# Kernel optimization log

Measured on AMD Instinct MI355X. Metric: run time of the kernel, lower is better.

## Reference

```python
import jax, jax.numpy as jnp
import numpy as np

PS = 32
D = 256


def setup_inputs() -> dict:
    key = jax.random.key(0)
    ks = jax.random.split(key, 9)
    B, L = 32, 32768
    s_in = 1.0 / np.sqrt(PS)
    s_d = 1.0 / np.sqrt(D)
    return {
        "x": jax.random.normal(ks[0], (B, L), dtype=jnp.float32),
        "W_proj": jax.random.normal(ks[1], (PS, D), dtype=jnp.float32) * s_in,
        "b_proj": jnp.zeros((D,), jnp.float32),
        "W_qkv": jax.random.normal(ks[2], (D, 3 * D), dtype=jnp.float32) * s_d,
        "b_qkv": jnp.zeros((3 * D,), jnp.float32),
        "W_out": jax.random.normal(ks[3], (D, D), dtype=jnp.float32) * s_d,
        "b_out": jnp.zeros((D,), jnp.float32),
        "W_head": jax.random.normal(ks[4], (D, PS), dtype=jnp.float32) * s_d,
        "b_head": jnp.zeros((PS,), jnp.float32),
    }


def reference(x, W_proj, b_proj, W_qkv, b_qkv, W_out, b_out, W_head, b_head):
    B, L = x.shape
    T = L // PS
    # InstanceNorm over full series (torch .std is unbiased -> ddof=1)
    mean = jnp.mean(x, axis=-1, keepdims=True)
    std = jnp.std(x, axis=-1, keepdims=True, ddof=1) + 1e-5
    x_norm = (x - mean) / std
    patches = x_norm.reshape(B, T, PS)
    # Patch embedding
    h = patches @ W_proj + b_proj  # [B, T, D]
    # Single-head causal self-attention (explicit scores, as in source)
    qkv = h @ W_qkv + b_qkv
    q, k, v = jnp.split(qkv, 3, axis=-1)
    scale = 1.0 / jnp.sqrt(jnp.asarray(D, dtype=h.dtype))
    attn = jnp.einsum("btd,bsd->bts", q, k) * scale  # [B, T, T]
    causal = jnp.tril(jnp.ones((T, T), dtype=bool))
    attn = jnp.where(causal, attn, -jnp.inf)
    attn = jax.nn.softmax(attn, axis=-1)
    out = jnp.einsum("bts,bsd->btd", attn, v)
    out = out @ W_out + b_out
    # Prediction head + next-patch MSE loss
    pred = out @ W_head + b_head  # [B, T, PS]
    loss = jnp.mean((pred[:, :-1] - patches[:, 1:]) ** 2)
    return loss
```

## Files before the change

kernel.cpp:

```cpp
#include <hip/hip_runtime.h>
#include <hip/hip_cooperative_groups.h>
#include <math.h>

namespace cg = cooperative_groups;

#define B_SZ 32
#define L_SZ 32768
#define T_SZ 1024
#define PS_SZ 32
#define D_SZ 256
#define SM_M 10.0f

typedef float f32x4 __attribute__((ext_vector_type(4)));
typedef short s16x8 __attribute__((ext_vector_type(8)));
typedef unsigned short u16x8 __attribute__((ext_vector_type(8)));

__device__ __forceinline__ unsigned short f2bf(float f) {
  union { float f; unsigned int u; } v; v.f = f;
  unsigned int r = v.u + 0x7FFFu + ((v.u >> 16) & 1u);
  return (unsigned short)(r >> 16);
}

__device__ __forceinline__ void g2l16(const unsigned short* g, unsigned short* l) {
  __builtin_amdgcn_global_load_lds(
      (const __attribute__((address_space(1))) unsigned int*)g,
      (__attribute__((address_space(3))) unsigned int*)l, 16, 0, 0);
}


__device__ __forceinline__ void phaseA_stats(const float* x, float* sgpart, int g, int tid,
                                             int w, int lane, float* red) {
  const int b = g >> 3;
  const float* p = x + (size_t)b * L_SZ + (size_t)(g & 7) * 4096;
  float s = 0.f, ss = 0.f;
#pragma unroll
  for (int i = 0; i < 4; ++i) {
    float4 f = ((const float4*)p)[tid + i * 256];
    s += f.x + f.y + f.z + f.w;
    ss += f.x * f.x + f.y * f.y + f.z * f.z + f.w * f.w;
  }
#pragma unroll
  for (int off = 32; off >= 1; off >>= 1) {
    s += __shfl_down(s, off);
    ss += __shfl_down(ss, off);
  }
  if (lane == 0) { red[w] = s; red[4 + w] = ss; }
  __syncthreads();
  if (tid == 0) {
    sgpart[g * 2]     = red[0] + red[1] + red[2] + red[3];
    sgpart[g * 2 + 1] = red[4] + red[5] + red[6] + red[7];
  }
  __syncthreads();
}

__device__ __forceinline__ void phaseA_folds(int idx, const float* Wp, const float* bp,
                                             const float* Wq, const float* bq,
                                             const float* Wo, const float* bo,
                                             const float* Wh, const float* bh,
                                             float* Wcb, unsigned short* WqT,
                                             unsigned short* WfT, float* bfp) {
  if (idx < 33 * 768) {
    int p = idx / 768, j = idx % 768;
    const float* arow = (p < 32) ? (Wp + p * 256) : bp;
    float acc = (p < 32) ? 0.f : bq[j];
    for (int d = 0; d < 256; ++d) acc += arow[d] * Wq[d * 768 + j];
    if (p < 32) WqT[j * 32 + p] = f2bf(acc);
    else Wcb[j] = acc;
  } else {
    int k = idx - 33 * 768;
    if (k < 8192) {
      int p = k >> 8, d = k & 255;
      float acc = 0.f;
      for (int e = 0; e < 256; ++e) acc += Wo[d * 256 + e] * Wh[e * 32 + p];
      WfT[p * 256 + d] = f2bf(acc);
    } else if (k < 8224) {
      int p = k - 8192;
      float acc = bh[p];
      for (int e = 0; e < 256; ++e) acc += bo[e] * Wh[e * 32 + p];
      bfp[p] = acc;
    }
  }
}

__device__ __forceinline__ void qkv_wave(const float* x, const float* sgpart,
                                         const unsigned short* WqT, const float* Wcb,
                                         unsigned short* Qb, unsigned short* Kb,
                                         unsigned short* Vtt, unsigned short* Tw,
                                         int mbase, int lane, int lo, int quad) {
  const int b = mbase >> 10;
  float S = 0.f, SS = 0.f;
#pragma unroll
  for (int i = 0; i < 8; ++i) {
    S += sgpart[(b * 8 + i) * 2];
    SS += sgpart[(b * 8 + i) * 2 + 1];
  }
  const float mean = S * (1.f / (float)L_SZ);
  const float var = (SS - S * mean) * (1.f / (float)(L_SZ - 1));
  const float inv = 1.f / (sqrtf(var) + 1e-5f);
  s16x8 af0, af1;
  {
    float4 a = *(const float4*)&x[(size_t)(mbase + lo) * 32 + quad * 8];
    float4 c = *(const float4*)&x[(size_t)(mbase + lo) * 32 + quad * 8 + 4];
    af0[0] = (short)f2bf((a.x - mean) * inv); af0[1] = (short)f2bf((a.y - mean) * inv);
    af0[2] = (short)f2bf((a.z - mean) * inv); af0[3] = (short)f2bf((a.w - mean) * inv);
    af0[4] = (short)f2bf((c.x - mean) * inv); af0[5] = (short)f2bf((c.y - mean) * inv);
    af0[6] = (short)f2bf((c.z - mean) * inv); af0[7] = (short)f2bf((c.w - mean) * inv);
    float4 d = *(const float4*)&x[(size_t)(mbase + 16 + lo) * 32 + quad * 8];
    float4 e = *(const float4*)&x[(size_t)(mbase + 16 + lo) * 32 + quad * 8 + 4];
    af1[0] = (short)f2bf((d.x - mean) * inv); af1[1] = (short)f2bf((d.y - mean) * inv);
    af1[2] = (short)f2bf((d.z - mean) * inv); af1[3] = (short)f2bf((d.w - mean) * inv);
    af1[4] = (short)f2bf((e.x - mean) * inv); af1[5] = (short)f2bf((e.y - mean) * inv);
    af1[6] = (short)f2bf((e.z - mean) * inv); af1[7] = (short)f2bf((e.w - mean) * inv);
  }
#pragma unroll 4
  for (int nt = 0; nt < 16; ++nt) {
    s16x8 bf = *(const s16x8*)&WqT[(size_t)(nt * 16 + lo) * 32 + quad * 8];
    f32x4 c0 = {0.f, 0.f, 0.f, 0.f}, c1 = {0.f, 0.f, 0.f, 0.f};
    c0 = __builtin_amdgcn_mfma_f32_16x16x32_bf16(af0, bf, c0, 0, 0, 0);
    c1 = __builtin_amdgcn_mfma_f32_16x16x32_bf16(af1, bf, c1, 0, 0, 0);
    const int col = nt * 16 + lo;
    const float bi = Wcb[col];
#pragma unroll
    for (int i = 0; i < 4; ++i) {
      Tw[(quad * 4 + i) * 264 + col]      = f2bf((c0[i] + bi) * 0.0625f);
      Tw[(16 + quad * 4 + i) * 264 + col] = f2bf((c1[i] + bi) * 0.0625f);
    }
  }
#pragma unroll
  for (int it = 0; it < 16; ++it) {
    const int gsub = it * 64 + lane;
    const int row = gsub >> 5, c16 = gsub & 31;
    *(u16x8*)&Qb[(size_t)(mbase + row) * 256 + c16 * 8] =
        *(const u16x8*)&Tw[row * 264 + c16 * 8];
  }
#pragma unroll 4
  for (int nt = 0; nt < 16; ++nt) {
    s16x8 bf = *(const s16x8*)&WqT[(size_t)(256 + nt * 16 + lo) * 32 + quad * 8];
    f32x4 c0 = {0.f, 0.f, 0.f, 0.f}, c1 = {0.f, 0.f, 0.f, 0.f};
    c0 = __builtin_amdgcn_mfma_f32_16x16x32_bf16(af0, bf, c0, 0, 0, 0);
    c1 = __builtin_amdgcn_mfma_f32_16x16x32_bf16(af1, bf, c1, 0, 0, 0);
    const int col = nt * 16 + lo;
    const float bi = Wcb[256 + col];
#pragma unroll
    for (int i = 0; i < 4; ++i) {
      Tw[(quad * 4 + i) * 264 + col]      = f2bf(c0[i] + bi);
      Tw[(16 + quad * 4 + i) * 264 + col] = f2bf(c1[i] + bi);
    }
  }
#pragma unroll
  for (int it = 0; it < 16; ++it) {
    const int gsub = it * 64 + lane;
    const int row = gsub >> 5, c16 = gsub & 31;
    *(u16x8*)&Kb[(size_t)(mbase + row) * 256 + c16 * 8] =
        *(const u16x8*)&Tw[row * 264 + c16 * 8];
  }
#pragma unroll 4
  for (int nt2 = 0; nt2 < 16; ++nt2) {
    s16x8 aw = *(const s16x8*)&WqT[(size_t)(512 + nt2 * 16 + lo) * 32 + quad * 8];
    f32x4 c0 = {0.f, 0.f, 0.f, 0.f}, c1 = {0.f, 0.f, 0.f, 0.f};
    c0 = __builtin_amdgcn_mfma_f32_16x16x32_bf16(aw, af0, c0, 0, 0, 0);
    c1 = __builtin_amdgcn_mfma_f32_16x16x32_bf16(aw, af1, c1, 0, 0, 0);
#pragma unroll
    for (int i = 0; i < 4; ++i) {
      const int d = nt2 * 16 + quad * 4 + i;
      const float bv = Wcb[512 + d];
      Tw[d * 32 + lo]      = f2bf(c0[i] + bv);
      Tw[d * 32 + 16 + lo] = f2bf(c1[i] + bv);
    }
  }
  {
    const int ktq = (mbase >> 5) & 31;
    const size_t vb = ((size_t)b * 32 + ktq) * 8192;
#pragma unroll
    for (int it = 0; it < 16; ++it) {
      const int gsub = it * 64 + lane;
      *(u16x8*)&Vtt[vb + gsub * 8] = *(const u16x8*)&Tw[gsub * 8];
    }
  }
}

__device__ __forceinline__ float attn_tile(const unsigned short* Qb,
                                           const unsigned short* Kb,
                                           const unsigned short* Vtt,
                                           const unsigned short* WfT, const float* bfp,
                                           const float* x, const float* sgpart,
                                           unsigned short* SMEM, int b, int qt,
                                           int tid, int w, int lane, int lo, int quad) {
  const int qr0 = qt * 64 + w * 16;
  const size_t kbase = (size_t)b << 10;

  s16x8 qf[8];
  const size_t qrow = (kbase + qr0 + lo) * 256;
#pragma unroll
  for (int kc = 0; kc < 8; ++kc) qf[kc] = *(const s16x8*)&Qb[qrow + kc * 32 + quad * 8];

  f32x4 O[16];
#pragma unroll
  for (int nt = 0; nt < 16; ++nt) O[nt] = (f32x4){0.f, 0.f, 0.f, 0.f};
  f32x4 Ol = {0.f, 0.f, 0.f, 0.f};
  s16x8 ones;
#pragma unroll
  for (int jj = 0; jj < 8; ++jj) ones[jj] = (short)0x3F80;

  const int c16p = tid & 31;
  const int keyr = tid >> 5;
  const int c16s = (c16p & 24) | ((c16p & 7) ^ keyr);
  const unsigned short* kgp = Kb + (kbase << 8) + keyr * 256 + c16s * 8;
  const int dql = tid >> 2;
  const int cpq = (tid & 3) ^ ((tid >> 3) & 3);
  const unsigned short* vgp = Vtt + (size_t)b * 262144 + dql * 32 + cpq * 8;

  unsigned short* myp = &SMEM[16384 + w * 640];
  const int lo7 = lo & 7;
  const int nk = 2 * (qt + 1);

  for (int kt = 0; kt < nk; ++kt) {
    const int k0 = kt * 32;
    __syncthreads();
#pragma unroll
    for (int it = 0; it < 4; ++it)
      g2l16(kgp + it * 2048, &SMEM[(it * 256 + w * 64) * 8]);
#pragma unroll
    for (int it = 0; it < 4; ++it)
      g2l16(vgp + it * 2048, &SMEM[8192 + (it * 256 + w * 64) * 8]);
    kgp += 8192; vgp += 8192;
    __syncthreads();

    if (k0 <= qr0 + 15) {
      f32x4 s0 = {0.f, 0.f, 0.f, 0.f}, s1 = {0.f, 0.f, 0.f, 0.f};
#pragma unroll
      for (int kc = 0; kc < 8; ++kc) {
        const int c16 = kc * 4 + quad;
        const int cs = (c16 & 24) | ((c16 & 7) ^ lo7);
        s16x8 kf0 = *(const s16x8*)&SMEM[(lo * 32 + cs) * 8];
        s16x8 kf1 = *(const s16x8*)&SMEM[((16 + lo) * 32 + cs) * 8];
        s0 = __builtin_amdgcn_mfma_f32_16x16x32_bf16(qf[kc], kf0, s0, 0, 0, 0);
        s1 = __builtin_amdgcn_mfma_f32_16x16x32_bf16(qf[kc], kf1, s1, 0, 0, 0);
      }
      if (k0 + 31 > qr0) {
#pragma unroll
        for (int ii = 0; ii < 4; ++ii) {
          const int row = qr0 + quad * 4 + ii;
          if (k0 + lo > row) s0[ii] = -1e30f;
          if (k0 + 16 + lo > row) s1[ii] = -1e30f;
        }
      }
#pragma unroll
      for (int ii = 0; ii < 4; ++ii) {
        myp[(quad * 4 + ii) * 40 + lo]      = f2bf(__expf(s0[ii] - SM_M));
        myp[(quad * 4 + ii) * 40 + 16 + lo] = f2bf(__expf(s1[ii] - SM_M));
      }
      s16x8 pf = *(const s16x8*)&myp[lo * 40 + quad * 8];
      Ol = __builtin_amdgcn_mfma_f32_16x16x32_bf16(pf, ones, Ol, 0, 0, 0);
#pragma unroll
      for (int nt = 0; nt < 16; ++nt) {
        const int d = nt * 16 + lo;
        const int cp = quad ^ ((d >> 1) & 3);
        s16x8 vf = *(const s16x8*)&SMEM[8192 + ((d << 2) + cp) * 8];
        O[nt] = __builtin_amdgcn_mfma_f32_16x16x32_bf16(pf, vf, O[nt], 0, 0, 0);
      }
    }
  }
  __syncthreads();

  float inv4[4];
#pragma unroll
  for (int ii = 0; ii < 4; ++ii) inv4[ii] = 1.f / Ol[ii];
  unsigned short* OLw = &SMEM[w * 4224];
#pragma unroll
  for (int nt = 0; nt < 16; ++nt)
#pragma unroll
    for (int ii = 0; ii < 4; ++ii)
      OLw[(quad * 4 + ii) * 264 + nt * 16 + lo] = f2bf(O[nt][ii] * inv4[ii]);

  s16x8 af[8];
#pragma unroll
  for (int kc = 0; kc < 8; ++kc)
    af[kc] = *(const s16x8*)&OLw[lo * 264 + kc * 32 + quad * 8];

  float S = 0.f, SS = 0.f;
#pragma unroll
  for (int i = 0; i < 8; ++i) {
    S += sgpart[(b * 8 + i) * 2];
    SS += sgpart[(b * 8 + i) * 2 + 1];
  }
  const float mean = S * (1.f / (float)L_SZ);
  const float var = (SS - S * mean) * (1.f / (float)(L_SZ - 1));
  const float invb = 1.f / (sqrtf(var) + 1e-5f);

  float lacc = 0.f;
#pragma unroll
  for (int nt = 0; nt < 2; ++nt) {
    f32x4 acc = {0.f, 0.f, 0.f, 0.f};
#pragma unroll
    for (int kc = 0; kc < 8; ++kc) {
      s16x8 bfr = *(const s16x8*)&WfT[(size_t)(nt * 16 + lo) * 256 + kc * 32 + quad * 8];
      acc = __builtin_amdgcn_mfma_f32_16x16x32_bf16(af[kc], bfr, acc, 0, 0, 0);
    }
    const float ba = bfp[nt * 16 + lo];
    const int p = nt * 16 + lo;
#pragma unroll
    for (int ii = 0; ii < 4; ++ii) {
      const int t = qr0 + quad * 4 + ii;
      if (t < 1023) {
        const float pr = acc[ii] + ba;
        const float tg = (x[(size_t)b * L_SZ + (t + 1) * 32 + p] - mean) * invb;
        const float d = pr - tg;
        lacc += d * d;
      }
    }
  }
#pragma unroll
  for (int off = 32; off >= 1; off >>= 1) lacc += __shfl_down(lacc, off);
  float* redf = (float*)&SMEM[17024];
  if (lane == 0) redf[w] = lacc;
  __syncthreads();
  return redf[0] + redf[1] + redf[2] + redf[3];
}

__global__ __launch_bounds__(256, 2) void mono_kernel(const float* __restrict__ x,
                                                      const float* __restrict__ Wp,
                                                      const float* __restrict__ bp,
                                                      const float* __restrict__ Wq,
                                                      const float* __restrict__ bq,
                                                      const float* __restrict__ Wo,
                                                      const float* __restrict__ bo,
                                                      const float* __restrict__ Wh,
                                                      const float* __restrict__ bh,
                                                      char* __restrict__ ws,
                                                      float* __restrict__ out) {
  __shared__ unsigned short SMEM[18944];

  unsigned short* Qb  = (unsigned short*)ws;
  unsigned short* Kb  = (unsigned short*)(ws + (16ull << 20));
  unsigned short* Vtt = (unsigned short*)(ws + (32ull << 20));
  char* tail = ws + (48ull << 20);
  float*          Wcb    = (float*)tail;
  unsigned short* WqT    = (unsigned short*)(tail + 4096);
  unsigned short* WfT    = (unsigned short*)(tail + 65536);
  float*          bfp    = (float*)(tail + 98304);
  float*          sgpart = (float*)(tail + 102400);
  float*          lossb  = (float*)(tail + 104448);

  const int g = blockIdx.x;
  const int tid = threadIdx.x;
  const int w = tid >> 6, lane = tid & 63;
  const int lo = lane & 15, quad = lane >> 4;
  cg::grid_group grid = cg::this_grid();

  if (g < 256) {
    phaseA_stats(x, sgpart, g, tid, w, lane, (float*)SMEM);
  } else if (g < 388) {
    phaseA_folds((g - 256) * 256 + tid, Wp, bp, Wq, bq, Wo, bo, Wh, bh, Wcb, WqT, WfT, bfp);
  }
  grid.sync();

  if (w < 2)
    qkv_wave(x, sgpart, WqT, Wcb, Qb, Kb, Vtt, &SMEM[w * 8448], g * 64 + w * 32, lane, lo, quad);
  grid.sync();

  {
    const int p_ = g & 255, copy = g >> 8;
    const int b = (p_ & 15) + copy * 16;
    const int qtv = p_ >> 4;
    const int qt = copy ? (15 - qtv) : qtv;
    float bl = attn_tile(Qb, Kb, Vtt, WfT, bfp, x, sgpart, SMEM, b, qt, tid, w, lane, lo, quad);
    if (tid == 0) lossb[g] = bl;
  }
  grid.sync();

  if (g == 0 && tid < 64) {
    float acc = 0.f;
#pragma unroll
    for (int i = 0; i < 8; ++i) acc += lossb[tid * 8 + i];
#pragma unroll
    for (int off = 32; off >= 1; off >>= 1) acc += __shfl_down(acc, off);
    if (tid == 0) out[0] = acc * (1.f / (float)(B_SZ * (T_SZ - 1) * PS_SZ));
  }
}

__global__ __launch_bounds__(256) void prep2_kernel(const float* __restrict__ x,
                                                    float* __restrict__ sgpart,
                                                    const float* __restrict__ Wp,
                                                    const float* __restrict__ bp,
                                                    const float* __restrict__ Wq,
                                                    const float* __restrict__ bq,
                                                    const float* __restrict__ Wo,
                                                    const float* __restrict__ bo,
                                                    const float* __restrict__ Wh,
                                                    const float* __restrict__ bh,
                                                    float* __restrict__ Wcb,
                                                    unsigned short* __restrict__ WqT,
                                                    unsigned short* __restrict__ WfT,
                                                    float* __restrict__ bfp,
                                                    float* __restrict__ lsum,
                                                    unsigned int* __restrict__ counter) {
  __shared__ float red[8];
  const int g = blockIdx.x, tid = threadIdx.x;
  const int w = tid >> 6, lane = tid & 63;
  if (g < 256) {
    phaseA_stats(x, sgpart, g, tid, w, lane, red);
  } else if (g < 388) {
    phaseA_folds((g - 256) * 256 + tid, Wp, bp, Wq, bq, Wo, bo, Wh, bh, Wcb, WqT, WfT, bfp);
  } else if (tid == 0) {
    lsum[0] = 0.f;
    counter[0] = 0u;
  }
}

__global__ __launch_bounds__(256) void qkv_kernel(const float* __restrict__ x,
                                                  const float* __restrict__ sgpart,
                                                  const unsigned short* __restrict__ WqT,
                                                  const float* __restrict__ Wcb,
                                                  unsigned short* __restrict__ Qb,
                                                  unsigned short* __restrict__ Kb,
                                                  unsigned short* __restrict__ Vtt) {
  __shared__ unsigned short T4[4][8448];
  const int tid = threadIdx.x;
  const int w = tid >> 6, lane = tid & 63;
  const int lo = lane & 15, quad = lane >> 4;
  qkv_wave(x, sgpart, WqT, Wcb, Qb, Kb, Vtt, T4[w], blockIdx.x * 128 + w * 32, lane, lo, quad);
}

__global__ __launch_bounds__(256) void attn2_kernel(const unsigned short* __restrict__ Qb,
                                                    const unsigned short* __restrict__ Kb,
                                                    const unsigned short* __restrict__ Vtt,
                                                    const unsigned short* __restrict__ WfT,
                                                    const float* __restrict__ bfp,
                                                    const float* __restrict__ x,
                                                    const float* __restrict__ sgpart,
                                                    float* __restrict__ lsum,
                                                    unsigned int* __restrict__ counter,
                                                    float* __restrict__ out) {
  __shared__ unsigned short SMEM[18944];
  const int g = blockIdx.x;
  const int j = g >> 3;
  const int b = (g & 7) * 4 + (j & 3);
  const int qt = 15 - (j >> 2);
  const int tid = threadIdx.x;
  const int w = tid >> 6, lane = tid & 63;
  const int lo = lane & 15, quad = lane >> 4;

  float bl = attn_tile(Qb, Kb, Vtt, WfT, bfp, x, sgpart, SMEM, b, qt, tid, w, lane, lo, quad);
  if (tid == 0) {
    atomicAdd(lsum, bl);
    __threadfence();
    unsigned int prev = atomicAdd(counter, 1u);
    if (prev == 511u) {
      float total = atomicAdd(lsum, 0.0f);
      out[0] = total * (1.f / (float)(B_SZ * (T_SZ - 1) * PS_SZ));
    }
  }
}

extern "C" void kernel_launch(void* const* d_in, const int* in_sizes, int n_in,
                              void* d_out, int out_size, void* d_ws, size_t ws_size,
                              hipStream_t stream) {
  const float* x      = (const float*)d_in[0];
  const float* W_proj = (const float*)d_in[1];
  const float* b_proj = (const float*)d_in[2];
  const float* W_qkv  = (const float*)d_in[3];
  const float* b_qkv  = (const float*)d_in[4];
  const float* W_out  = (const float*)d_in[5];
  const float* b_out  = (const float*)d_in[6];
  const float* W_head = (const float*)d_in[7];
  const float* b_head = (const float*)d_in[8];
  float* out = (float*)d_out;
  char* ws = (char*)d_ws;

  char* tail = ws + (48ull << 20);
  unsigned short* Qb     = (unsigned short*)ws;
  unsigned short* Kb     = (unsigned short*)(ws + (16ull << 20));
  unsigned short* Vtt    = (unsigned short*)(ws + (32ull << 20));
  float*          Wcb    = (float*)tail;
  unsigned short* WqT    = (unsigned short*)(tail + 4096);
  unsigned short* WfT    = (unsigned short*)(tail + 65536);
  float*          bfp    = (float*)(tail + 98304);
  float*          sgpart = (float*)(tail + 102400);
  float*          lsum   = (float*)(tail + 106496);
  unsigned int*   counter = (unsigned int*)(tail + 106752);

  int maxb = 0;
  hipError_t oe = hipOccupancyMaxActiveBlocksPerMultiprocessor(&maxb, mono_kernel, 256, 0);
  bool coop_ok = (oe == hipSuccess) && (maxb >= 2);

  if (coop_ok) {
    void* args[] = {(void*)&x, (void*)&W_proj, (void*)&b_proj, (void*)&W_qkv, (void*)&b_qkv,
                    (void*)&W_out, (void*)&b_out, (void*)&W_head, (void*)&b_head,
                    (void*)&ws, (void*)&out};
    hipError_t le = hipLaunchCooperativeKernel((const void*)mono_kernel, dim3(512), dim3(256),
                                               args, 0, stream);
    if (le == hipSuccess) return;
    (void)hipGetLastError();
  }

  prep2_kernel<<<389, 256, 0, stream>>>(x, sgpart, W_proj, b_proj, W_qkv, b_qkv,
                                        W_out, b_out, W_head, b_head,
                                        Wcb, WqT, WfT, bfp, lsum, counter);
  qkv_kernel<<<256, 256, 0, stream>>>(x, sgpart, WqT, Wcb, Qb, Kb, Vtt);
  attn2_kernel<<<512, 256, 0, stream>>>(Qb, Kb, Vtt, WfT, bfp, x, sgpart, lsum, counter, out);
}
```

Measured before the change: 168.4 us.

## Replace cooperative grid syncs with per-batch flag sync between QKV and attention

Drops the cooperative mono kernel with its three grid-wide barriers. Work now runs as a prep kernel plus one fused kernel, in which every block computes a 64-row slice of QKV for its batch, raises a per-batch counter, and spins until all 16 slices of that batch are done before running attention. The final loss is reduced by the last block to finish, using an atomic ticket. This replaces global barriers with batch-local dependencies so attention can start as soon as its batch is ready. The spin-wait relies on all 512 blocks being resident at once, which is not guaranteed without a cooperative launch and could deadlock.

```diff
diff --git a/kernel.cpp b/kernel.cpp
--- a/kernel.cpp
+++ b/kernel.cpp
@@ -1,8 +1,5 @@
 #include <hip/hip_runtime.h>
-#include <hip/hip_cooperative_groups.h>
 #include <math.h>
-
-namespace cg = cooperative_groups;
 
 #define B_SZ 32
 #define L_SZ 32768
@@ -27,7 +24,6 @@
       (__attribute__((address_space(3))) unsigned int*)l, 16, 0, 0);
 }
 
-
 __device__ __forceinline__ void phaseA_stats(const float* x, float* sgpart, int g, int tid,
                                              int w, int lane, float* red) {
   const int b = g >> 3;
@@ -50,7 +46,6 @@
     sgpart[g * 2]     = red[0] + red[1] + red[2] + red[3];
     sgpart[g * 2 + 1] = red[4] + red[5] + red[6] + red[7];
   }
-  __syncthreads();
 }
 
 __device__ __forceinline__ void phaseA_folds(int idx, const float* Wp, const float* bp,
@@ -82,100 +77,30 @@
   }
 }
 
-__device__ __forceinline__ void qkv_wave(const float* x, const float* sgpart,
-                                         const unsigned short* WqT, const float* Wcb,
-                                         unsigned short* Qb, unsigned short* Kb,
-                                         unsigned short* Vtt, unsigned short* Tw,
-                                         int mbase, int lane, int lo, int quad) {
-  const int b = mbase >> 10;
-  float S = 0.f, SS = 0.f;
-#pragma unroll
-  for (int i = 0; i < 8; ++i) {
-    S += sgpart[(b * 8 + i) * 2];
-    SS += sgpart[(b * 8 + i) * 2 + 1];
-  }
-  const float mean = S * (1.f / (float)L_SZ);
-  const float var = (SS - S * mean) * (1.f / (float)(L_SZ - 1));
-  const float inv = 1.f / (sqrtf(var) + 1e-5f);
-  s16x8 af0, af1;
-  {
-    float4 a = *(const float4*)&x[(size_t)(mbase + lo) * 32 + quad * 8];
-    float4 c = *(const float4*)&x[(size_t)(mbase + lo) * 32 + quad * 8 + 4];
-    af0[0] = (short)f2bf((a.x - mean) * inv); af0[1] = (short)f2bf((a.y - mean) * inv);
-    af0[2] = (short)f2bf((a.z - mean) * inv); af0[3] = (short)f2bf((a.w - mean) * inv);
-    af0[4] = (short)f2bf((c.x - mean) * inv); af0[5] = (short)f2bf((c.y - mean) * inv);
-    af0[6] = (short)f2bf((c.z - mean) * inv); af0[7] = (short)f2bf((c.w - mean) * inv);
-    float4 d = *(const float4*)&x[(size_t)(mbase + 16 + lo) * 32 + quad * 8];
-    float4 e = *(const float4*)&x[(size_t)(mbase + 16 + lo) * 32 + quad * 8 + 4];
-    af1[0] = (short)f2bf((d.x - mean) * inv); af1[1] = (short)f2bf((d.y - mean) * inv);
-    af1[2] = (short)f2bf((d.z - mean) * inv); af1[3] = (short)f2bf((d.w - mean) * inv);
-    af1[4] = (short)f2bf((e.x - mean) * inv); af1[5] = (short)f2bf((e.y - mean) * inv);
-    af1[6] = (short)f2bf((e.z - mean) * inv); af1[7] = (short)f2bf((e.w - mean) * inv);
-  }
-#pragma unroll 4
-  for (int nt = 0; nt < 16; ++nt) {
-    s16x8 bf = *(const s16x8*)&WqT[(size_t)(nt * 16 + lo) * 32 + quad * 8];
-    f32x4 c0 = {0.f, 0.f, 0.f, 0.f}, c1 = {0.f, 0.f, 0.f, 0.f};
-    c0 = __builtin_amdgcn_mfma_f32_16x16x32_bf16(af0, bf, c0, 0, 0, 0);
-    c1 = __builtin_amdgcn_mfma_f32_16x16x32_bf16(af1, bf, c1, 0, 0, 0);
-    const int col = nt * 16 + lo;
-    const float bi = Wcb[col];
-#pragma unroll
-    for (int i = 0; i < 4; ++i) {
-      Tw[(quad * 4 + i) * 264 + col]      = f2bf((c0[i] + bi) * 0.0625f);
-      Tw[(16 + quad * 4 + i) * 264 + col] = f2bf((c1[i] + bi) * 0.0625f);
-    }
-  }
-#pragma unroll
-  for (int it = 0; it < 16; ++it) {
-    const int gsub = it * 64 + lane;
-    const int row = gsub >> 5, c16 = gsub & 31;
-    *(u16x8*)&Qb[(size_t)(mbase + row) * 256 + c16 * 8] =
-        *(const u16x8*)&Tw[row * 264 + c16 * 8];
-  }
-#pragma unroll 4
-  for (int nt = 0; nt < 16; ++nt) {
-    s16x8 bf = *(const s16x8*)&WqT[(size_t)(256 + nt * 16 + lo) * 32 + quad * 8];
-    f32x4 c0 = {0.f, 0.f, 0.f, 0.f}, c1 = {0.f, 0.f, 0.f, 0.f};
-    c0 = __builtin_amdgcn_mfma_f32_16x16x32_bf16(af0, bf, c0, 0, 0, 0);
-    c1 = __builtin_amdgcn_mfma_f32_16x16x32_bf16(af1, bf, c1, 0, 0, 0);
-    const int col = nt * 16 + lo;
-    const float bi = Wcb[256 + col];
-#pragma unroll
-    for (int i = 0; i < 4; ++i) {
-      Tw[(quad * 4 + i) * 264 + col]      = f2bf(c0[i] + bi);
-      Tw[(16 + quad * 4 + i) * 264 + col] = f2bf(c1[i] + bi);
-    }
-  }
-#pragma unroll
-  for (int it = 0; it < 16; ++it) {
-    const int gsub = it * 64 + lane;
-    const int row = gsub >> 5, c16 = gsub & 31;
-    *(u16x8*)&Kb[(size_t)(mbase + row) * 256 + c16 * 8] =
-        *(const u16x8*)&Tw[row * 264 + c16 * 8];
-  }
-#pragma unroll 4
-  for (int nt2 = 0; nt2 < 16; ++nt2) {
-    s16x8 aw = *(const s16x8*)&WqT[(size_t)(512 + nt2 * 16 + lo) * 32 + quad * 8];
-    f32x4 c0 = {0.f, 0.f, 0.f, 0.f}, c1 = {0.f, 0.f, 0.f, 0.f};
-    c0 = __builtin_amdgcn_mfma_f32_16x16x32_bf16(aw, af0, c0, 0, 0, 0);
-    c1 = __builtin_amdgcn_mfma_f32_16x16x32_bf16(aw, af1, c1, 0, 0, 0);
-#pragma unroll
-    for (int i = 0; i < 4; ++i) {
-      const int d = nt2 * 16 + quad * 4 + i;
-      const float bv = Wcb[512 + d];
-      Tw[d * 32 + lo]      = f2bf(c0[i] + bv);
-      Tw[d * 32 + 16 + lo] = f2bf(c1[i] + bv);
-    }
-  }
-  {
-    const int ktq = (mbase >> 5) & 31;
-    const size_t vb = ((size_t)b * 32 + ktq) * 8192;
-#pragma unroll
-    for (int it = 0; it < 16; ++it) {
-      const int gsub = it * 64 + lane;
-      *(u16x8*)&Vtt[vb + gsub * 8] = *(const u16x8*)&Tw[gsub * 8];
-    }
+__global__ __launch_bounds__(256) void prep_kernel(const float* __restrict__ x,
+                                                   float* __restrict__ sgpart,
+                                                   const float* __restrict__ Wp,
+                                                   const float* __restrict__ bp,
+                                                   const float* __restrict__ Wq,
+                                                   const float* __restrict__ bq,
+                                                   const float* __restrict__ Wo,
+                                                   const float* __restrict__ bo,
+                                                   const float* __restrict__ Wh,
+                                                   const float* __restrict__ bh,
+                                                   float* __restrict__ Wcb,
+                                                   unsigned short* __restrict__ WqT,
+                                                   unsigned short* __restrict__ WfT,
+                                                   float* __restrict__ bfp,
+                                                   unsigned int* __restrict__ ctrs) {
+  __shared__ float red[8];
+  const int g = blockIdx.x, tid = threadIdx.x;
+  const int w = tid >> 6, lane = tid & 63;
+  if (g < 256) {
+    phaseA_stats(x, sgpart, g, tid, w, lane, red);
+  } else if (g < 388) {
+    phaseA_folds((g - 256) * 256 + tid, Wp, bp, Wq, bq, Wo, bo, Wh, bh, Wcb, WqT, WfT, bfp);
+  } else {
+    if (tid < 33) ctrs[tid] = 0u;
   }
 }
 
@@ -318,138 +243,140 @@
   return redf[0] + redf[1] + redf[2] + redf[3];
 }
 
-__global__ __launch_bounds__(256, 2) void mono_kernel(const float* __restrict__ x,
-                                                      const float* __restrict__ Wp,
-                                                      const float* __restrict__ bp,
-                                                      const float* __restrict__ Wq,
-                                                      const float* __restrict__ bq,
-                                                      const float* __restrict__ Wo,
-                                                      const float* __restrict__ bo,
-                                                      const float* __restrict__ Wh,
-                                                      const float* __restrict__ bh,
-                                                      char* __restrict__ ws,
-                                                      float* __restrict__ out) {
+__global__ __launch_bounds__(256, 2) void fused_kernel(const float* __restrict__ x,
+                                                       const float* __restrict__ sgpart,
+                                                       const unsigned short* __restrict__ WqT,
+                                                       const float* __restrict__ Wcb,
+                                                       const unsigned short* __restrict__ WfT,
+                                                       const float* __restrict__ bfp,
+                                                       unsigned short* __restrict__ Qb,
+                                                       unsigned short* __restrict__ Kb,
+                                                       unsigned short* __restrict__ Vtt,
+                                                       unsigned int* __restrict__ done_b,
+                                                       unsigned int* __restrict__ total,
+                                                       float* __restrict__ lossb,
+                                                       float* __restrict__ out) {
   __shared__ unsigned short SMEM[18944];
-
-  unsigned short* Qb  = (unsigned short*)ws;
-  unsigned short* Kb  = (unsigned short*)(ws + (16ull << 20));
-  unsigned short* Vtt = (unsigned short*)(ws + (32ull << 20));
-  char* tail = ws + (48ull << 20);
-  float*          Wcb    = (float*)tail;
-  unsigned short* WqT    = (unsigned short*)(tail + 4096);
-  unsigned short* WfT    = (unsigned short*)(tail + 65536);
-  float*          bfp    = (float*)(tail + 98304);
-  float*          sgpart = (float*)(tail + 102400);
-  float*          lossb  = (float*)(tail + 104448);
-
   const int g = blockIdx.x;
   const int tid = threadIdx.x;
   const int w = tid >> 6, lane = tid & 63;
   const int lo = lane & 15, quad = lane >> 4;
-  cg::grid_group grid = cg::this_grid();
-
-  if (g < 256) {
-    phaseA_stats(x, sgpart, g, tid, w, lane, (float*)SMEM);
-  } else if (g < 388) {
-    phaseA_folds((g - 256) * 256 + tid, Wp, bp, Wq, bq, Wo, bo, Wh, bh, Wcb, WqT, WfT, bfp);
-  }
-  grid.sync();
-
-  if (w < 2)
-    qkv_wave(x, sgpart, WqT, Wcb, Qb, Kb, Vtt, &SMEM[w * 8448], g * 64 + w * 32, lane, lo, quad);
-  grid.sync();
+
+  const int bq = (g & 7) * 4 + ((g >> 3) & 3);
+  const int chunk = g >> 5;
+  const int r0 = bq * 1024 + chunk * 64 + w * 16;
 
   {
-    const int p_ = g & 255, copy = g >> 8;
-    const int b = (p_ & 15) + copy * 16;
-    const int qtv = p_ >> 4;
-    const int qt = copy ? (15 - qtv) : qtv;
-    float bl = attn_tile(Qb, Kb, Vtt, WfT, bfp, x, sgpart, SMEM, b, qt, tid, w, lane, lo, quad);
-    if (tid == 0) lossb[g] = bl;
-  }
-  grid.sync();
-
-  if (g == 0 && tid < 64) {
+    float S = 0.f, SS = 0.f;
+#pragma unroll
+    for (int i = 0; i < 8; ++i) {
+      S += sgpart[(bq * 8 + i) * 2];
+      SS += sgpart[(bq * 8 + i) * 2 + 1];
+    }
+    const float mean = S * (1.f / (float)L_SZ);
+    const float var = (SS - S * mean) * (1.f / (float)(L_SZ - 1));
+    const float inv = 1.f / (sqrtf(var) + 1e-5f);
+    unsigned short* Tw = &SMEM[w * 4224];
+
+    s16x8 af0;
+    {
+      float4 a = *(const float4*)&x[(size_t)(r0 + lo) * 32 + quad * 8];
+      float4 c = *(const float4*)&x[(size_t)(r0 + lo) * 32 + quad * 8 + 4];
+      af0[0] = (short)f2bf((a.x - mean) * inv); af0[1] = (short)f2bf((a.y - mean) * inv);
+      af0[2] = (short)f2bf((a.z - mean) * inv); af0[3] = (short)f2bf((a.w - mean) * inv);
+      af0[4] = (short)f2bf((c.x - mean) * inv); af0[5] = (short)f2bf((c.y - mean) * inv);
+      af0[6] = (short)f2bf((c.z - mean) * inv); af0[7] = (short)f2bf((c.w - mean) * inv);
+    }
+#pragma unroll 4
+    for (int nt = 0; nt < 16; ++nt) {
+      s16x8 bf = *(const s16x8*)&WqT[(size_t)(nt * 16 + lo) * 32 + quad * 8];
+      f32x4 c0 = {0.f, 0.f, 0.f, 0.f};
+      c0 = __builtin_amdgcn_mfma_f32_16x16x32_bf16(af0, bf, c0, 0, 0, 0);
+      const int col = nt * 16 + lo;
+      const float bi = Wcb[col];
+#pragma unroll
+      for (int i = 0; i < 4; ++i)
+        Tw[(quad * 4 + i) * 264 + col] = f2bf((c0[i] + bi) * 0.0625f);
+    }
+#pragma unroll
+    for (int it = 0; it < 8; ++it) {
+      const int c = it * 64 + lane;
+      const int row = c >> 5, c16 = c & 31;
+      *(u16x8*)&Qb[(size_t)(r0 + row) * 256 + c16 * 8] = *(const u16x8*)&Tw[row * 264 + c16 * 8];
+    }
+#pragma unroll 4
+    for (int nt = 0; nt < 16; ++nt) {
+      s16x8 bf = *(const s16x8*)&WqT[(size_t)(256 + nt * 16 + lo) * 32 + quad * 8];
+      f32x4 c0 = {0.f, 0.f, 0.f, 0.f};
+      c0 = __builtin_amdgcn_mfma_f32_16x16x32_bf16(af0, bf, c0, 0, 0, 0);
+      const int col = nt * 16 + lo;
+      const float bi = Wcb[256 + col];
+#pragma unroll
+      for (int i = 0; i < 4; ++i)
+        Tw[(quad * 4 + i) * 264 + col] = f2bf(c0[i] + bi);
+    }
+#pragma unroll
+    for (int it = 0; it < 8; ++it) {
+      const int c = it * 64 + lane;
+      const int row = c >> 5, c16 = c & 31;
+      *(u16x8*)&Kb[(size_t)(r0 + row) * 256 + c16 * 8] = *(const u16x8*)&Tw[row * 264 + c16 * 8];
+    }
+#pragma unroll 4
+    for (int nt2 = 0; nt2 < 16; ++nt2) {
+      s16x8 aw = *(const s16x8*)&WqT[(size_t)(512 + nt2 * 16 + lo) * 32 + quad * 8];
+      f32x4 c0 = {0.f, 0.f, 0.f, 0.f};
+      c0 = __builtin_amdgcn_mfma_f32_16x16x32_bf16(aw, af0, c0, 0, 0, 0);
+#pragma unroll
+      for (int i = 0; i < 4; ++i) {
+        const int d = nt2 * 16 + quad * 4 + i;
+        Tw[d * 16 + lo] = f2bf(c0[i] + Wcb[512 + d]);
+      }
+    }
+    {
+      const int ktq = chunk * 2 + (w >> 1);
+      const int tb = (w & 1) * 16;
+      const size_t vb = ((size_t)bq * 32 + ktq) * 8192;
+#pragma unroll
+      for (int it = 0; it < 8; ++it) {
+        const int c = it * 64 + lane;
+        const int d = c >> 1, half = c & 1;
+        *(u16x8*)&Vtt[vb + d * 32 + tb + half * 8] = *(const u16x8*)&Tw[d * 16 + half * 8];
+      }
+    }
+  }
+  __threadfence();
+  __syncthreads();
+  if (tid == 0) atomicAdd(&done_b[bq], 1u);
+
+  const int qt = (g >> 8) ? (15 - ((g >> 5) & 7)) : ((g >> 5) & 7);
+  if (tid == 0) {
+    while (atomicAdd(&done_b[bq], 0u) < 16u) __builtin_amdgcn_s_sleep(8);
+  }
+  __syncthreads();
+  __threadfence();
+
+  float bl = attn_tile(Qb, Kb, Vtt, WfT, bfp, x, sgpart, SMEM, bq, qt, tid, w, lane, lo, quad);
+
+  unsigned int* flag = (unsigned int*)&SMEM[17100];
+  if (tid == 0) {
+    lossb[g] = bl;
+    __threadfence();
+    unsigned int prev = atomicAdd(total, 1u);
+    flag[0] = (prev == 511u) ? 1u : 0u;
+  }
+  __syncthreads();
+  if (flag[0]) {
+    __threadfence();
     float acc = 0.f;
-#pragma unroll
-    for (int i = 0; i < 8; ++i) acc += lossb[tid * 8 + i];
+    for (int i = tid; i < 512; i += 256) acc += atomicAdd(&lossb[i], 0.0f);
 #pragma unroll
     for (int off = 32; off >= 1; off >>= 1) acc += __shfl_down(acc, off);
-    if (tid == 0) out[0] = acc * (1.f / (float)(B_SZ * (T_SZ - 1) * PS_SZ));
-  }
-}
-
-__global__ __launch_bounds__(256) void prep2_kernel(const float* __restrict__ x,
-                                                    float* __restrict__ sgpart,
-                                                    const float* __restrict__ Wp,
-                                                    const float* __restrict__ bp,
-                                                    const float* __restrict__ Wq,
-                                                    const float* __restrict__ bq,
-                                                    const float* __restrict__ Wo,
-                                                    const float* __restrict__ bo,
-                                                    const float* __restrict__ Wh,
-                                                    const float* __restrict__ bh,
-                                                    float* __restrict__ Wcb,
-                                                    unsigned short* __restrict__ WqT,
-                                                    unsigned short* __restrict__ WfT,
-                                                    float* __restrict__ bfp,
-                                                    float* __restrict__ lsum,
-                                                    unsigned int* __restrict__ counter) {
-  __shared__ float red[8];
-  const int g = blockIdx.x, tid = threadIdx.x;
-  const int w = tid >> 6, lane = tid & 63;
-  if (g < 256) {
-    phaseA_stats(x, sgpart, g, tid, w, lane, red);
-  } else if (g < 388) {
-    phaseA_folds((g - 256) * 256 + tid, Wp, bp, Wq, bq, Wo, bo, Wh, bh, Wcb, WqT, WfT, bfp);
-  } else if (tid == 0) {
-    lsum[0] = 0.f;
-    counter[0] = 0u;
-  }
-}
-
-__global__ __launch_bounds__(256) void qkv_kernel(const float* __restrict__ x,
-                                                  const float* __restrict__ sgpart,
-                                                  const unsigned short* __restrict__ WqT,
-                                                  const float* __restrict__ Wcb,
-                                                  unsigned short* __restrict__ Qb,
-                                                  unsigned short* __restrict__ Kb,
-                                                  unsigned short* __restrict__ Vtt) {
-  __shared__ unsigned short T4[4][8448];
-  const int tid = threadIdx.x;
-  const int w = tid >> 6, lane = tid & 63;
-  const int lo = lane & 15, quad = lane >> 4;
-  qkv_wave(x, sgpart, WqT, Wcb, Qb, Kb, Vtt, T4[w], blockIdx.x * 128 + w * 32, lane, lo, quad);
-}
-
-__global__ __launch_bounds__(256) void attn2_kernel(const unsigned short* __restrict__ Qb,
-                                                    const unsigned short* __restrict__ Kb,
-                                                    const unsigned short* __restrict__ Vtt,
-                                                    const unsigned short* __restrict__ WfT,
-                                                    const float* __restrict__ bfp,
-                                                    const float* __restrict__ x,
-                                                    const float* __restrict__ sgpart,
-                                                    float* __restrict__ lsum,
-                                                    unsigned int* __restrict__ counter,
-                                                    float* __restrict__ out) {
-  __shared__ unsigned short SMEM[18944];
-  const int g = blockIdx.x;
-  const int j = g >> 3;
-  const int b = (g & 7) * 4 + (j & 3);
-  const int qt = 15 - (j >> 2);
-  const int tid = threadIdx.x;
-  const int w = tid >> 6, lane = tid & 63;
-  const int lo = lane & 15, quad = lane >> 4;
-
-  float bl = attn_tile(Qb, Kb, Vtt, WfT, bfp, x, sgpart, SMEM, b, qt, tid, w, lane, lo, quad);
-  if (tid == 0) {
-    atomicAdd(lsum, bl);
-    __threadfence();
-    unsigned int prev = atomicAdd(counter, 1u);
-    if (prev == 511u) {
-      float total = atomicAdd(lsum, 0.0f);
-      out[0] = total * (1.f / (float)(B_SZ * (T_SZ - 1) * PS_SZ));
-    }
+    float* redf = (float*)&SMEM[17200];
+    if (lane == 0) redf[w] = acc;
+    __syncthreads();
+    if (tid == 0)
+      out[0] = (redf[0] + redf[1] + redf[2] + redf[3]) *
+               (1.f / (float)(B_SZ * (T_SZ - 1) * PS_SZ));
   }
 }
 
@@ -468,35 +395,22 @@
   float* out = (float*)d_out;
   char* ws = (char*)d_ws;
 
-  char* tail = ws + (48ull << 20);
   unsigned short* Qb     = (unsigned short*)ws;
   unsigned short* Kb     = (unsigned short*)(ws + (16ull << 20));
   unsigned short* Vtt    = (unsigned short*)(ws + (32ull << 20));
+  char* tail = ws + (48ull << 20);
   float*          Wcb    = (float*)tail;
   unsigned short* WqT    = (unsigned short*)(tail + 4096);
   unsigned short* WfT    = (unsigned short*)(tail + 65536);
   float*          bfp    = (float*)(tail + 98304);
   float*          sgpart = (float*)(tail + 102400);
-  float*          lsum   = (float*)(tail + 106496);
-  unsigned int*   counter = (unsigned int*)(tail + 106752);
-
-  int maxb = 0;
-  hipError_t oe = hipOccupancyMaxActiveBlocksPerMultiprocessor(&maxb, mono_kernel, 256, 0);
-  bool coop_ok = (oe == hipSuccess) && (maxb >= 2);
-
-  if (coop_ok) {
-    void* args[] = {(void*)&x, (void*)&W_proj, (void*)&b_proj, (void*)&W_qkv, (void*)&b_qkv,
-                    (void*)&W_out, (void*)&b_out, (void*)&W_head, (void*)&b_head,
-                    (void*)&ws, (void*)&out};
-    hipError_t le = hipLaunchCooperativeKernel((const void*)mono_kernel, dim3(512), dim3(256),
-                                               args, 0, stream);
-    if (le == hipSuccess) return;
-    (void)hipGetLastError();
-  }
-
-  prep2_kernel<<<389, 256, 0, stream>>>(x, sgpart, W_proj, b_proj, W_qkv, b_qkv,
-                                        W_out, b_out, W_head, b_head,
-                                        Wcb, WqT, WfT, bfp, lsum, counter);
-  qkv_kernel<<<256, 256, 0, stream>>>(x, sgpart, WqT, Wcb, Qb, Kb, Vtt);
-  attn2_kernel<<<512, 256, 0, stream>>>(Qb, Kb, Vtt, WfT, bfp, x, sgpart, lsum, counter, out);
-}
+  unsigned int*   done_b = (unsigned int*)(tail + 106496);
+  unsigned int*   total  = (unsigned int*)(tail + 106496 + 128);
+  float*          lossb  = (float*)(tail + 106752);
+
+  prep_kernel<<<389, 256, 0, stream>>>(x, sgpart, W_proj, b_proj, W_qkv, b_qkv,
+                                       W_out, b_out, W_head, b_head,
+                                       Wcb, WqT, WfT, bfp, done_b);
+  fused_kernel<<<512, 256, 0, stream>>>(x, sgpart, WqT, Wcb, WfT, bfp,
+                                        Qb, Kb, Vtt, done_b, total, lossb, out);
+}
```

Measured after the change: 288.5 us. 1.71x slower.
